# Optimization experiments

Hardware: AMD Instinct MI355X
Metric: run time of the kernel (lower is better)

Reference implementation:

```python
import jax, jax.numpy as jnp
from jax import lax
import numpy as np


def _conv2d(x, w, pad, dil=1):
    return lax.conv_general_dilated(x, w, (1, 1), [(pad, pad), (pad, pad)],
                                    rhs_dilation=(dil, dil),
                                    dimension_numbers=('NCHW', 'OIHW', 'NCHW'))


def _conv1d(x, w):
    # x [B,C,L], w [O,I,K], 'same' padding
    k = w.shape[2]
    return lax.conv_general_dilated(x, w, (1,), [(k // 2, k // 2)],
                                    dimension_numbers=('NCH', 'OIH', 'NCH'))


def _scan_fwd(slices, w):
    # slices [L,B,C,M]; s[i] += relu(conv1d(s[i-1])) for i=1..L-1 (sequential, carries updates)
    def f(c, r):
        n = r + jax.nn.relu(_conv1d(c, w))
        return n, n
    _, out = lax.scan(f, slices[0], slices[1:])
    return jnp.concatenate([slices[:1], out], axis=0)


def _scan_bwd(slices, w):
    # s[i] += relu(conv1d(s[i+1])) for i = L-2 .. 1 (first and last slice untouched)
    def f(c, r):
        n = r + jax.nn.relu(_conv1d(c, w))
        return n, n
    _, out = lax.scan(f, slices[-1], slices[-2:0:-1])
    return jnp.concatenate([slices[:1], out[::-1], slices[-1:]], axis=0)


def _resize_bilinear_ac(x, oh, ow):
    # bilinear, align_corners=True, x [B,C,H,W]
    H, W = x.shape[2], x.shape[3]
    ys = jnp.linspace(0.0, H - 1.0, oh)
    xs = jnp.linspace(0.0, W - 1.0, ow)
    y0 = jnp.floor(ys).astype(jnp.int32); y1 = jnp.minimum(y0 + 1, H - 1)
    x0 = jnp.floor(xs).astype(jnp.int32); x1 = jnp.minimum(x0 + 1, W - 1)
    wy = (ys - y0)[:, None]
    wx = xs - x0
    r = x[:, :, y0, :] * (1.0 - wy) + x[:, :, y1, :] * wy  # [B,C,oh,W]
    return r[:, :, :, x0] * (1.0 - wx) + r[:, :, :, x1] * wx


def reference(x, w11, s11, b11, w12, s12, b12, w21, s21, b21, w22, s22, b22,
              w31, s31, b31, w32, s32, b32, w33, s33, b33,
              w41, s41, b41, w42, s42, b42, w43, s43, b43,
              w51, s51, b51, w52, s52, b52, w53, s53, b53,
              w6, s6, b6, w7, s7, b7, wd, wu, wr, wl, w8, b8,
              fw9, fb9, fw10, fb10):
    def cbr(h, w, s, b, pad=1, dil=1):
        y = _conv2d(h, w, pad, dil)
        return jax.nn.relu(y * s[None, :, None, None] + b[None, :, None, None])

    def mp(h):
        B, C, H, W = h.shape
        return h.reshape(B, C, H // 2, 2, W // 2, 2).max((3, 5))

    x = cbr(x, w11, s11, b11); x = cbr(x, w12, s12, b12); x = mp(x)
    x = cbr(x, w21, s21, b21); x = cbr(x, w22, s22, b22); x = mp(x)
    x = cbr(x, w31, s31, b31); x = cbr(x, w32, s32, b32); x = cbr(x, w33, s33, b33); x = mp(x)
    x = cbr(x, w41, s41, b41); x = cbr(x, w42, s42, b42); x = cbr(x, w43, s43, b43)
    x = cbr(x, w51, s51, b51, pad=2, dil=2)
    x = cbr(x, w52, s52, b52, pad=2, dil=2)
    x = cbr(x, w53, s53, b53, pad=2, dil=2)
    x = cbr(x, w6, s6, b6, pad=4, dil=4)
    x = cbr(x, w7, s7, b7, pad=0)

    # SCNN spatial message passing (down, up over rows; right, left over cols)
    rows = jnp.moveaxis(x, 2, 0)            # [H,B,C,W]
    rows = _scan_fwd(rows, wd[:, :, 0, :])  # down
    rows = _scan_bwd(rows, wu[:, :, 0, :])  # up
    x = jnp.moveaxis(rows, 0, 2)
    cols = jnp.moveaxis(x, 3, 0)            # [W,B,C,H]
    cols = _scan_fwd(cols, wr[:, :, :, 0])  # right
    cols = _scan_bwd(cols, wl[:, :, :, 0])  # left
    x = jnp.moveaxis(cols, 0, 3)

    # dropout2d(p=0.1) treated as identity (deterministic/eval reference)
    x = _conv2d(x, w8, 0) + b8[None, :, None, None]  # [B,5,36,100]

    x1 = jax.nn.softmax(_resize_bilinear_ac(x, 288, 800), axis=1)

    x2 = jax.nn.softmax(x, axis=1)
    B, C, H, W = x2.shape
    x2 = x2.reshape(B, C, H // 2, 2, W // 2, 2).mean((3, 5)).reshape(B, -1)
    x2 = jax.nn.relu(x2 @ fw9.T + fb9)
    x2 = jax.nn.sigmoid(x2 @ fw10.T + fb10)
    return (x1, x2)


def setup_inputs():
    key = jax.random.key(0)
    ks = iter(jax.random.split(key, 80))

    def conv_w(ci, co, kh, kw):
        return jax.random.normal(next(ks), (co, ci, kh, kw), jnp.float32) * np.float32(np.sqrt(2.0 / (ci * kh * kw)))

    def bn(c):
        s = 0.9 + 0.2 * jax.random.uniform(next(ks), (c,), jnp.float32)
        b = 0.1 * jax.random.normal(next(ks), (c,), jnp.float32)
        return s, b

    d = {}
    d['x'] = jax.random.normal(next(ks), (4, 3, 288, 800), jnp.float32)
    specs = [('11', 3, 64), ('12', 64, 64), ('21', 64, 128), ('22', 128, 128),
             ('31', 128, 256), ('32', 256, 256), ('33', 256, 256),
             ('41', 256, 512), ('42', 512, 512), ('43', 512, 512),
             ('51', 512, 512), ('52', 512, 512), ('53', 512, 512)]
    for n, ci, co in specs:
        d['w' + n] = conv_w(ci, co, 3, 3)
        d['s' + n], d['b' + n] = bn(co)
    d['w6'] = conv_w(512, 1024, 3, 3); d['s6'], d['b6'] = bn(1024)
    d['w7'] = conv_w(1024, 128, 1, 1); d['s7'], d['b7'] = bn(128)
    # small scale keeps the 100-step additive recurrence numerically tame
    for n, (kh, kw) in (('wd', (1, 9)), ('wu', (1, 9)), ('wr', (9, 1)), ('wl', (9, 1))):
        d[n] = jax.random.normal(next(ks), (128, 128, kh, kw), jnp.float32) * 0.001
    d['w8'] = conv_w(128, 5, 1, 1)
    d['b8'] = 0.1 * jax.random.normal(next(ks), (5,), jnp.float32)
    d['fw9'] = jax.random.normal(next(ks), (128, 4500), jnp.float32) / np.float32(np.sqrt(4500.0))
    d['fb9'] = jnp.zeros((128,), jnp.float32)
    d['fw10'] = jax.random.normal(next(ks), (4, 128), jnp.float32) / np.float32(np.sqrt(128.0))
    d['fb10'] = jnp.zeros((4,), jnp.float32)
    return d
```

## Files before the change

kernel.cpp:

```cpp
#include <hip/hip_runtime.h>
#include <math.h>


#define NB 4

typedef unsigned short ushort_t;
typedef __attribute__((ext_vector_type(8))) short short8x;
typedef __attribute__((ext_vector_type(4))) float facc4;

static __device__ __forceinline__ ushort_t f2bh(float x) {
    unsigned u = __float_as_uint(x);
    unsigned r = u + 0x7fffu + ((u >> 16) & 1u);
    return (ushort_t)(r >> 16);
}
static __device__ __forceinline__ float bh2f(ushort_t h) {
    return __uint_as_float(((unsigned)h) << 16);
}
static __device__ __forceinline__ void split_store(float v, ushort_t* __restrict__ hi,
                                                   ushort_t* __restrict__ lo, size_t idx) {
    ushort_t h = f2bh(v);
    float l = v - bh2f(h);
    hi[idx] = h;
    lo[idx] = f2bh(l);
}
static __device__ __forceinline__ void ld8f(const float* p, float f[8]) {
    float4 a = *(const float4*)p;
    float4 b = *(const float4*)(p + 4);
    f[0] = a.x; f[1] = a.y; f[2] = a.z; f[3] = a.w;
    f[4] = b.x; f[5] = b.y; f[6] = b.z; f[7] = b.w;
}

__global__ __launch_bounds__(256) void repack_w_k(const float* __restrict__ w, float* __restrict__ wre,
                                                  int O, int IK) {
    int gid = blockIdx.x * 256 + threadIdx.x;
    if (gid >= O * IK) return;
    int o = gid / IK;
    int r = gid - o * IK;
    wre[r * O + o] = w[gid];
}

__global__ __launch_bounds__(256) void conv11_strip_k(const float* __restrict__ X0, const float* __restrict__ W11,
                                                      const float* __restrict__ sc, const float* __restrict__ bi,
                                                      ushort_t* __restrict__ Thi, ushort_t* __restrict__ Tlo, int r0) {
    int gid = blockIdx.x * 256 + threadIdx.x;
    if (gid >= 4 * 20 * 802 * 8) return;
    int c8 = gid & 7;
    int t = gid >> 3;
    int w = t % 802; t /= 802;
    int tr = t % 20;
    int b = t / 20;
    int gr = r0 - 1 + tr;
    int gc = w - 1;
    size_t obase = (((size_t)b * 20 + tr) * 802 + w) * 64 + c8 * 8;
    if (gr < 0 || gr >= 288 || gc < 0 || gc >= 800) {
#pragma unroll
        for (int j = 0; j < 8; ++j) { Thi[obase + j] = 0; Tlo[obase + j] = 0; }
        return;
    }
    float acc[8];
#pragma unroll
    for (int j = 0; j < 8; ++j) acc[j] = 0.f;
#pragma unroll
    for (int ci = 0; ci < 3; ++ci) {
        const float* inc = X0 + (size_t)(b * 3 + ci) * 288 * 800;
#pragma unroll
        for (int kh = 0; kh < 3; ++kh) {
            int ih = gr + kh - 1;
            if (ih < 0 || ih >= 288) continue;
#pragma unroll
            for (int kw = 0; kw < 3; ++kw) {
                int iw = gc + kw - 1;
                if (iw < 0 || iw >= 800) continue;
                float v = inc[ih * 800 + iw];
                float wf[8];
                ld8f(W11 + (ci * 9 + kh * 3 + kw) * 64 + c8 * 8, wf);
#pragma unroll
                for (int j = 0; j < 8; ++j) acc[j] = fmaf(v, wf[j], acc[j]);
            }
        }
    }
#pragma unroll
    for (int j = 0; j < 8; ++j) {
        int n = c8 * 8 + j;
        float r = acc[j] * sc[n] + bi[n];
        r = r > 0.f ? r : 0.f;
        split_store(r, Thi, Tlo, obase + j);
    }
}

__global__ __launch_bounds__(256) void repack_wmfma_k(const float* __restrict__ w, ushort_t* __restrict__ whi,
                                                      ushort_t* __restrict__ wlo, int N, int Cin, int taps) {
    int gid = blockIdx.x * 256 + threadIdx.x;
    if (gid >= N * Cin * taps) return;
    int o = gid / (Cin * taps);
    int r = gid - o * Cin * taps;
    int i = r / taps;
    int t = r - i * taps;
    float x = w[gid];
    size_t d = ((size_t)t * N + o) * Cin + i;
    ushort_t h = f2bh(x);
    whi[d] = h;
    wlo[d] = f2bh(x - bh2f(h));
}

__global__ __launch_bounds__(256) void vpool2_k(const ushort_t* __restrict__ shi, const ushort_t* __restrict__ slo,
                                                ushort_t* __restrict__ dhi, ushort_t* __restrict__ dlo,
                                                int Hs, int Wp, int C, int Hop, int Wop, int pad, int pr0) {
    int total = 4 * (Hs >> 1) * Wp * C;
    int gid = blockIdx.x * 256 + threadIdx.x;
    if (gid >= total) return;
    int c = gid % C;
    int t = gid / C;
    int w = t % Wp; t /= Wp;
    int hp = t % (Hs >> 1);
    int b = t / (Hs >> 1);
    size_t a0 = (((size_t)b * Hs + 2 * hp) * Wp + w) * C + c;
    size_t a1 = a0 + (size_t)Wp * C;
    float v0 = bh2f(shi[a0]) + bh2f(slo[a0]);
    float v1 = bh2f(shi[a1]) + bh2f(slo[a1]);
    float v = fmaxf(v0, v1);
    size_t d = (((size_t)b * Hop + pr0 + hp + pad) * Wop + (w + pad)) * C + c;
    split_store(v, dhi, dlo, d);
}

template <int MODE, int NJ>
__global__ __launch_bounds__(256) void mfma_conv_k(
    const ushort_t* __restrict__ Ahi, const ushort_t* __restrict__ Alo,
    const ushort_t* __restrict__ Whi, const ushort_t* __restrict__ Wlo,
    const float* __restrict__ sc, const float* __restrict__ bi,
    ushort_t* __restrict__ Ohi, ushort_t* __restrict__ Olo, float* __restrict__ Fo,
    int M, int Wimg, int HS, int h0,
    int HpIn, int WpIn, int Cin, int ih0, int iph, int ipw, int dil, int taps,
    int N, int obst, int oh0, int oph, int opw, int WpOut) {
    constexpr int NT = NJ * 32;
    __shared__ ushort_t sA0[128 * 40], sA1[128 * 40];
    __shared__ ushort_t sB0[NT * 40], sB1[NT * 40];

    int tid = threadIdx.x;
    int m0 = blockIdx.x * 128;
    int n0 = blockIdx.y * NT;

    int ar = tid >> 1;
    int ah = (tid & 1) * 16;
    int am = m0 + ar;
    if (am >= M) am = M - 1;
    int aw = am % Wimg;
    int t1 = am / Wimg;
    int ahh = h0 + t1 % HS;
    int ab = t1 / HS;

    int br, bhh, bpl;
    if (NJ == 4) {
        br = tid >> 1; bhh = (tid & 1) * 16; bpl = 2;
    } else {
        int bp = tid >> 7;
        int bidx = tid & 127;
        br = bidx >> 1; bhh = (bidx & 1) * 16; bpl = bp;
    }

    int wid = tid >> 6, lane = tid & 63;
    int moff = (wid >> 1) * 64;
    int noff = (wid & 1) * (NJ * 16);
    int lm = lane & 15, quad = lane >> 4;

    facc4 acc[4][NJ];
#pragma unroll
    for (int i = 0; i < 4; ++i)
#pragma unroll
        for (int j = 0; j < NJ; ++j) acc[i][j] = (facc4)(0.f);

    for (int t = 0; t < taps; ++t) {
        int dh = 0, dw = 0;
        if (taps == 9) {
            dh = (t / 3 - 1) * dil;
            dw = (t % 3 - 1) * dil;
        }
        size_t aoff = (((size_t)ab * HpIn + (ahh - ih0 + iph + dh)) * WpIn + (aw + ipw + dw)) * Cin + ah;
        size_t boff0 = ((size_t)t * N + (n0 + br)) * Cin + bhh;
        for (int k0 = 0; k0 < Cin; k0 += 32) {
            {
                const ushort_t* p = Ahi + aoff + k0;
                uint4 v0 = *(const uint4*)p;
                uint4 v1 = *(const uint4*)(p + 8);
                *(uint4*)&sA0[ar * 40 + ah] = v0;
                *(uint4*)&sA0[ar * 40 + ah + 8] = v1;
                const ushort_t* q = Alo + aoff + k0;
                uint4 w0 = *(const uint4*)q;
                uint4 w1 = *(const uint4*)(q + 8);
                *(uint4*)&sA1[ar * 40 + ah] = w0;
                *(uint4*)&sA1[ar * 40 + ah + 8] = w1;
            }
            if (NJ == 4) {
                const ushort_t* p = Whi + boff0 + k0;
                uint4 v0 = *(const uint4*)p;
                uint4 v1 = *(const uint4*)(p + 8);
                *(uint4*)&sB0[br * 40 + bhh] = v0;
                *(uint4*)&sB0[br * 40 + bhh + 8] = v1;
                const ushort_t* q = Wlo + boff0 + k0;
                uint4 w0 = *(const uint4*)q;
                uint4 w1 = *(const uint4*)(q + 8);
                *(uint4*)&sB1[br * 40 + bhh] = w0;
                *(uint4*)&sB1[br * 40 + bhh + 8] = w1;
            } else {
                const ushort_t* p = (bpl ? Wlo : Whi) + boff0 + k0;
                uint4 v0 = *(const uint4*)p;
                uint4 v1 = *(const uint4*)(p + 8);
                ushort_t* dst = bpl ? sB1 : sB0;
                *(uint4*)&dst[br * 40 + bhh] = v0;
                *(uint4*)&dst[br * 40 + bhh + 8] = v1;
            }
            __syncthreads();
            short8x afh[4], afl[4], bfh[NJ], bfl[NJ];
#pragma unroll
            for (int mi = 0; mi < 4; ++mi) {
                int base = (moff + mi * 16 + lm) * 40 + quad * 8;
                afh[mi] = *(const short8x*)&sA0[base];
                afl[mi] = *(const short8x*)&sA1[base];
            }
#pragma unroll
            for (int nj = 0; nj < NJ; ++nj) {
                int base = (noff + nj * 16 + lm) * 40 + quad * 8;
                bfh[nj] = *(const short8x*)&sB0[base];
                bfl[nj] = *(const short8x*)&sB1[base];
            }
#pragma unroll
            for (int mi = 0; mi < 4; ++mi)
#pragma unroll
                for (int nj = 0; nj < NJ; ++nj) {
                    acc[mi][nj] = __builtin_amdgcn_mfma_f32_16x16x32_bf16(afh[mi], bfh[nj], acc[mi][nj], 0, 0, 0);
                    acc[mi][nj] = __builtin_amdgcn_mfma_f32_16x16x32_bf16(afl[mi], bfh[nj], acc[mi][nj], 0, 0, 0);
                    acc[mi][nj] = __builtin_amdgcn_mfma_f32_16x16x32_bf16(afh[mi], bfl[nj], acc[mi][nj], 0, 0, 0);
                }
            __syncthreads();
        }
    }

#pragma unroll
    for (int mi = 0; mi < 4; ++mi)
#pragma unroll
        for (int nj = 0; nj < NJ; ++nj) {
            int nglob = n0 + noff + nj * 16 + lm;
            float s = sc[nglob];
            float bb = bi[nglob];
            if (MODE == 1) {
#pragma unroll
                for (int rg = 0; rg < 4; rg += 2) {
                    int mg = m0 + moff + mi * 16 + quad * 4 + rg;
                    if (mg >= M) continue;
                    float v0 = acc[mi][nj][rg] * s + bb;
                    v0 = v0 > 0.f ? v0 : 0.f;
                    float v1 = acc[mi][nj][rg + 1] * s + bb;
                    v1 = v1 > 0.f ? v1 : 0.f;
                    float v = fmaxf(v0, v1);
                    int wq = mg % Wimg;
                    int tq = mg / Wimg;
                    int hq = h0 + tq % HS;
                    int bq = tq / HS;
                    size_t a = ((size_t)bq * obst + (size_t)(hq - oh0) * WpOut + (wq >> 1)) * N + nglob;
                    split_store(v, Ohi, Olo, a);
                }
            } else {
#pragma unroll
                for (int rg = 0; rg < 4; ++rg) {
                    int mg = m0 + moff + mi * 16 + quad * 4 + rg;
                    if (mg >= M) continue;
                    float v = acc[mi][nj][rg] * s + bb;
                    v = v > 0.f ? v : 0.f;
                    int wq = mg % Wimg;
                    int tq = mg / Wimg;
                    int hq = h0 + tq % HS;
                    int bq = tq / HS;
                    if (MODE == 0) {
                        size_t a = ((size_t)bq * obst + (size_t)(hq - oh0 + oph) * WpOut + (wq + opw)) * N + nglob;
                        split_store(v, Ohi, Olo, a);
                    } else {
                        size_t a = (((size_t)bq * N + nglob) * HS + (hq - h0)) * Wimg + wq;
                        Fo[a] = v;
                    }
                }
            }
        }
}

__global__ __launch_bounds__(256) void repack_scan_k(const float* __restrict__ w, float* __restrict__ wre) {
    int gid = blockIdx.x * 256 + threadIdx.x;
    if (gid >= 128 * 128 * 9) return;
    int o = gid / 1152;
    int r = gid - o * 1152;
    wre[r * 128 + o] = w[gid];
}

__global__ __launch_bounds__(256) void scan_row_k(float* __restrict__ F, const float* __restrict__ wsc, int hp, int hc) {
    __shared__ float sm[128 * 12];
    int b = blockIdx.x / 25;
    int w0 = (blockIdx.x % 25) * 4;
    int tid = threadIdx.x;
    const float* Fp = F + ((size_t)(b * 128) * 36 + hp) * 100;
    for (int i = tid; i < 1536; i += 256) {
        int ci = i / 12;
        int j = i - ci * 12;
        int iw = w0 - 4 + j;
        sm[i] = (iw >= 0 && iw < 100) ? Fp[(size_t)ci * 3600 + iw] : 0.f;
    }
    __syncthreads();
    int o = tid & 127;
    int half = tid >> 7;
    float a0 = 0.f, a1 = 0.f;
    for (int ci = 0; ci < 128; ++ci) {
        const float* s = sm + ci * 12 + half * 2;
        const float* wp = wsc + ci * 9 * 128 + o;
#pragma unroll
        for (int k = 0; k < 9; ++k) {
            float wt = wp[k * 128];
            a0 = fmaf(s[k], wt, a0);
            a1 = fmaf(s[k + 1], wt, a1);
        }
    }
    int w = w0 + half * 2;
    float* outp = F + ((size_t)(b * 128 + o) * 36 + hc) * 100 + w;
    outp[0] += a0 > 0.f ? a0 : 0.f;
    outp[1] += a1 > 0.f ? a1 : 0.f;
}

__global__ __launch_bounds__(256) void scan_colT_k(float* __restrict__ FT, const float* __restrict__ wsc, int wp_, int wc) {
    __shared__ float sm[128 * 12];
    int b = blockIdx.x / 9;
    int h0 = (blockIdx.x % 9) * 4;
    int tid = threadIdx.x;
    const float* Fp = FT + (size_t)(b * 128) * 3600 + (size_t)wp_ * 36;
    for (int i = tid; i < 1536; i += 256) {
        int ci = i / 12;
        int j = i - ci * 12;
        int ih = h0 - 4 + j;
        sm[i] = (ih >= 0 && ih < 36) ? Fp[(size_t)ci * 3600 + ih] : 0.f;
    }
    __syncthreads();
    int o = tid & 127;
    int half = tid >> 7;
    float a0 = 0.f, a1 = 0.f;
    for (int ci = 0; ci < 128; ++ci) {
        const float* s = sm + ci * 12 + half * 2;
        const float* wp = wsc + ci * 9 * 128 + o;
#pragma unroll
        for (int k = 0; k < 9; ++k) {
            float wt = wp[k * 128];
            a0 = fmaf(s[k], wt, a0);
            a1 = fmaf(s[k + 1], wt, a1);
        }
    }
    int h = h0 + half * 2;
    float* outp = FT + ((size_t)(b * 128 + o) * 100 + wc) * 36 + h;
    outp[0] += a0 > 0.f ? a0 : 0.f;
    outp[1] += a1 > 0.f ? a1 : 0.f;
}

__global__ __launch_bounds__(256) void transpose_fwd_k(const float* __restrict__ F, float* __restrict__ FT) {
    int gid = blockIdx.x * 256 + threadIdx.x;
    if (gid >= 4 * 128 * 3600) return;
    int h = gid % 36;
    int t = gid / 36;
    int w = t % 100;
    int bc = t / 100;
    FT[gid] = F[(size_t)bc * 3600 + h * 100 + w];
}
__global__ __launch_bounds__(256) void transpose_bwd_k(const float* __restrict__ FT, float* __restrict__ F) {
    int gid = blockIdx.x * 256 + threadIdx.x;
    if (gid >= 4 * 128 * 3600) return;
    int w = gid % 100;
    int t = gid / 100;
    int h = t % 36;
    int bc = t / 36;
    F[gid] = FT[(size_t)bc * 3600 + w * 36 + h];
}

__global__ __launch_bounds__(256) void conv8_k(const float* __restrict__ F, const float* __restrict__ w8,
                                               const float* __restrict__ b8, float* __restrict__ G) {
    int gid = blockIdx.x * 256 + threadIdx.x;
    if (gid >= NB * 3600) return;
    int hw = gid % 3600;
    int b = gid / 3600;
    float acc[5];
#pragma unroll
    for (int c = 0; c < 5; ++c) acc[c] = b8[c];
    const float* Fb = F + (size_t)b * 128 * 3600 + hw;
    for (int ci = 0; ci < 128; ++ci) {
        float v = Fb[(size_t)ci * 3600];
#pragma unroll
        for (int c = 0; c < 5; ++c) acc[c] = fmaf(v, w8[c * 128 + ci], acc[c]);
    }
#pragma unroll
    for (int c = 0; c < 5; ++c) G[(size_t)(b * 5 + c) * 3600 + hw] = acc[c];
}

__global__ __launch_bounds__(256) void resize_softmax_k(const float* __restrict__ G, float* __restrict__ out) {
    int gid = blockIdx.x * 256 + threadIdx.x;
    if (gid >= NB * 288 * 800) return;
    int ox = gid % 800;
    int t = gid / 800;
    int oy = t % 288;
    int b = t / 288;
    float fy = oy * (35.0f / 287.0f);
    int y0 = (int)fy; if (y0 > 34) y0 = 34;
    int y1 = y0 + 1;
    float wy = fy - y0;
    float fx = ox * (99.0f / 799.0f);
    int x0 = (int)fx; if (x0 > 98) x0 = 98;
    int x1 = x0 + 1;
    float wx = fx - x0;
    const float* Gb = G + (size_t)b * 5 * 3600;
    float v[5];
    float m = -1e30f;
#pragma unroll
    for (int c = 0; c < 5; ++c) {
        const float* Gc = Gb + (size_t)c * 3600;
        float a = Gc[y0 * 100 + x0] * (1.f - wx) + Gc[y0 * 100 + x1] * wx;
        float bb = Gc[y1 * 100 + x0] * (1.f - wx) + Gc[y1 * 100 + x1] * wx;
        v[c] = a * (1.f - wy) + bb * wy;
        m = fmaxf(m, v[c]);
    }
    float sum = 0.f;
#pragma unroll
    for (int c = 0; c < 5; ++c) { v[c] = expf(v[c] - m); sum += v[c]; }
    float inv = 1.f / sum;
#pragma unroll
    for (int c = 0; c < 5; ++c) out[((size_t)(b * 5 + c) * 288 + oy) * 800 + ox] = v[c] * inv;
}

__global__ __launch_bounds__(256) void pool_softmax_k(const float* __restrict__ G, float* __restrict__ P) {
    int gid = blockIdx.x * 256 + threadIdx.x;
    if (gid >= NB * 18 * 50) return;
    int pw = gid % 50;
    int t = gid / 50;
    int ph = t % 18;
    int b = t / 18;
    float s5[5] = {0.f, 0.f, 0.f, 0.f, 0.f};
    const float* Gb = G + (size_t)b * 5 * 3600;
#pragma unroll
    for (int dy = 0; dy < 2; ++dy) {
#pragma unroll
        for (int dx = 0; dx < 2; ++dx) {
            int hw = (2 * ph + dy) * 100 + (2 * pw + dx);
            float v[5], m = -1e30f, sum = 0.f;
#pragma unroll
            for (int c = 0; c < 5; ++c) { v[c] = Gb[(size_t)c * 3600 + hw]; m = fmaxf(m, v[c]); }
#pragma unroll
            for (int c = 0; c < 5; ++c) { v[c] = expf(v[c] - m); sum += v[c]; }
            float inv = 1.f / sum;
#pragma unroll
            for (int c = 0; c < 5; ++c) s5[c] += v[c] * inv;
        }
    }
#pragma unroll
    for (int c = 0; c < 5; ++c) P[b * 4500 + c * 900 + ph * 50 + pw] = s5[c] * 0.25f;
}

__global__ __launch_bounds__(256) void fc1_k(const float* __restrict__ P, const float* __restrict__ fw9,
                                             const float* __restrict__ fb9, float* __restrict__ H1) {
    int wid = blockIdx.x * 4 + (threadIdx.x >> 6);
    int lane = threadIdx.x & 63;
    if (wid >= 512) return;
    int b = wid >> 7;
    int o = wid & 127;
    const float* wr = fw9 + (size_t)o * 4500;
    const float* pr = P + b * 4500;
    float acc = 0.f;
    for (int i = lane; i < 4500; i += 64) acc = fmaf(wr[i], pr[i], acc);
    for (int s = 32; s > 0; s >>= 1) acc += __shfl_down(acc, s, 64);
    if (lane == 0) {
        float r = acc + fb9[o];
        H1[b * 128 + o] = r > 0.f ? r : 0.f;
    }
}

__global__ __launch_bounds__(64) void fc2_k(const float* __restrict__ H1, const float* __restrict__ fw10,
                                            const float* __restrict__ fb10, float* __restrict__ dout) {
    int t = threadIdx.x;
    if (t >= 16) return;
    int b = t >> 2;
    int o = t & 3;
    float acc = fb10[o];
    for (int i = 0; i < 128; ++i) acc = fmaf(H1[b * 128 + i], fw10[o * 128 + i], acc);
    dout[4608000 + t] = 1.f / (1.f + expf(-acc));
}

static inline int ceildiv(int a, int b) { return (a + b - 1) / b; }

extern "C" void kernel_launch(void* const* d_in, const int* in_sizes, int n_in,
                              void* d_out, int out_size, void* d_ws, size_t ws_size,
                              hipStream_t stream) {
    (void)in_sizes; (void)n_in; (void)out_size; (void)ws_size;
    char* U = (char*)d_ws;
    char* V = U + 19000064;

    float* W11f = (float*)(U);
    ushort_t* WM12 = (ushort_t*)(U + 8192);
    ushort_t* WM21 = (ushort_t*)(U + 155648);
    ushort_t* WM22 = (ushort_t*)(U + 450560);
    ushort_t* T1hi = (ushort_t*)(U + 1050624);
    ushort_t* T1lo = (ushort_t*)(U + 1050624 + 8212480);
    ushort_t* T3hi = (ushort_t*)(U + 1050624);
    ushort_t* T3lo = (ushort_t*)(U + 1050624 + 8232960);
    ushort_t* WMa = (ushort_t*)(U);
    ushort_t* WMb = (ushort_t*)(U + 4718592);
    float* WSC = (float*)(U);
    float* G = (float*)(U + 2359296);
    float* P = (float*)(U + 2647296);
    float* H1 = (float*)(U + 2719296);

    ushort_t* Xhi = (ushort_t*)(V);
    ushort_t* Xlo = (ushort_t*)(V + 15306752);
    ushort_t* S1hi = (ushort_t*)(V + 30613504);
    ushort_t* S1lo = (ushort_t*)(V + 60663808);
    ushort_t* T2hi = (ushort_t*)(V + 90714112);
    ushort_t* T2lo = (ushort_t*)(V + 90714112 + 3686400);
    ushort_t* Yhi = (ushort_t*)(V + 30613504);
    ushort_t* Ylo = (ushort_t*)(V + 61227008);
    ushort_t* Zhi = (ushort_t*)(V + 91840512);
    ushort_t* Zlo = (ushort_t*)(V + 97632256);
    ushort_t* HPhi = (ushort_t*)(V);
    ushort_t* HPlo = (ushort_t*)(V + 14745600);
    ushort_t* PAhi = (ushort_t*)(V + 30613504);
    ushort_t* PAlo = (ushort_t*)(V + 40345600);
    ushort_t* SBhi = (ushort_t*)(V + 50077696);
    ushort_t* SBlo = (ushort_t*)(V + 69541888);
    ushort_t* SAhi = (ushort_t*)(V);
    ushort_t* SAlo = (ushort_t*)(V + 19464192);
    ushort_t* C6hi = (ushort_t*)(V + 38928384);
    ushort_t* C6lo = (ushort_t*)(V + 68419584);
    float* F = (float*)(V);
    float* FT = (float*)(V + 7372800);

    const float* X0 = (const float*)d_in[0];
    auto din = [&](int i) { return (const float*)d_in[i]; };
    auto wm_lo = [&](ushort_t* base, int taps, int N, int C) { return base + (size_t)taps * N * C; };

    repack_w_k<<<ceildiv(27 * 64, 256), 256, 0, stream>>>(din(1), W11f, 64, 27);
    repack_wmfma_k<<<ceildiv(64 * 64 * 9, 256), 256, 0, stream>>>(din(4), WM12, wm_lo(WM12, 9, 64, 64), 64, 64, 9);
    hipMemsetAsync(V + 30613504, 0, 60100608, stream);
    for (int s = 0; s < 16; ++s) {
        int r0 = s * 18;
        conv11_strip_k<<<2005, 256, 0, stream>>>(X0, W11f, din(2), din(3), T1hi, T1lo, r0);
        mfma_conv_k<1, 2><<<dim3(450, 1), 256, 0, stream>>>(
            T1hi, T1lo, WM12, wm_lo(WM12, 9, 64, 64), din(5), din(6), T2hi, T2lo, nullptr,
            57600, 800, 18, r0, 20, 802, 64, r0, 1, 1, 1, 9, 64, 18 * 400, r0, 0, 0, 400);
        vpool2_k<<<ceildiv(4 * 9 * 400 * 64, 256), 256, 0, stream>>>(
            T2hi, T2lo, S1hi, S1lo, 18, 400, 64, 146, 402, 1, r0 / 2);
    }
    repack_wmfma_k<<<ceildiv(128 * 64 * 9, 256), 256, 0, stream>>>(din(7), WM21, wm_lo(WM21, 9, 128, 64), 128, 64, 9);
    repack_wmfma_k<<<ceildiv(128 * 128 * 9, 256), 256, 0, stream>>>(din(10), WM22, wm_lo(WM22, 9, 128, 128), 128, 128, 9);
    hipMemsetAsync(V, 0, 30613504, stream);
    for (int s = 0; s < 8; ++s) {
        int r0 = s * 18;
        int hstart = r0 - 1 < 0 ? 0 : r0 - 1;
        int hend = r0 + 19 > 144 ? 144 : r0 + 19;
        int rows = hend - hstart;
        int M21 = 4 * rows * 400;
        hipMemsetAsync(U + 1050624, 0, 16465920, stream);
        mfma_conv_k<0, 4><<<dim3(ceildiv(M21, 128), 1), 256, 0, stream>>>(
            S1hi, S1lo, WM21, wm_lo(WM21, 9, 128, 64), din(8), din(9), T3hi, T3lo, nullptr,
            M21, 400, rows, hstart, 146, 402, 64, 0, 1, 1, 1, 9, 128, 20 * 402, r0 - 1, 0, 1, 402);
        mfma_conv_k<1, 4><<<dim3(225, 1), 256, 0, stream>>>(
            T3hi, T3lo, WM22, wm_lo(WM22, 9, 128, 128), din(11), din(12), T2hi, T2lo, nullptr,
            28800, 400, 18, r0, 20, 402, 128, r0 - 1, 0, 1, 1, 9, 128, 18 * 200, r0, 0, 0, 200);
        vpool2_k<<<ceildiv(4 * 9 * 200 * 128, 256), 256, 0, stream>>>(
            T2hi, T2lo, Xhi, Xlo, 18, 200, 128, 74, 202, 1, r0 / 2);
    }

    repack_wmfma_k<<<ceildiv(256 * 128 * 9, 256), 256, 0, stream>>>(din(13), WMa, wm_lo(WMa, 9, 256, 128), 256, 128, 9);
    hipMemsetAsync(V + 30613504, 0, 61227008, stream);
    mfma_conv_k<0, 4><<<dim3(450, 2), 256, 0, stream>>>(
        Xhi, Xlo, WMa, wm_lo(WMa, 9, 256, 128), din(14), din(15), Yhi, Ylo, nullptr,
        57600, 200, 72, 0, 74, 202, 128, 0, 1, 1, 1, 9, 256, 74 * 202, 0, 1, 1, 202);
    repack_wmfma_k<<<ceildiv(256 * 256 * 9, 256), 256, 0, stream>>>(din(16), WMa, wm_lo(WMa, 9, 256, 256), 256, 256, 9);
    repack_wmfma_k<<<ceildiv(256 * 256 * 9, 256), 256, 0, stream>>>(din(19), WMb, wm_lo(WMb, 9, 256, 256), 256, 256, 9);
    for (int s = 0; s < 6; ++s) {
        int h0s = s * 12;
        int hstart = h0s - 1 < 0 ? 0 : h0s - 1;
        int hend = h0s + 13 > 72 ? 72 : h0s + 13;
        int rows = hend - hstart;
        int M32 = 4 * rows * 200;
        hipMemsetAsync(V + 91840512, 0, 11583488, stream);
        mfma_conv_k<0, 4><<<dim3(ceildiv(M32, 128), 2), 256, 0, stream>>>(
            Yhi, Ylo, WMa, wm_lo(WMa, 9, 256, 256), din(17), din(18), Zhi, Zlo, nullptr,
            M32, 200, rows, hstart, 74, 202, 256, 0, 1, 1, 1, 9, 256, 14 * 202, h0s - 1, 0, 1, 202);
        mfma_conv_k<1, 4><<<dim3(75, 2), 256, 0, stream>>>(
            Zhi, Zlo, WMb, wm_lo(WMb, 9, 256, 256), din(20), din(21), HPhi, HPlo, nullptr,
            9600, 200, 12, h0s, 14, 202, 256, h0s - 1, 0, 1, 1, 9, 256, 72 * 100, 0, 0, 0, 100);
    }
    hipMemsetAsync(V + 30613504, 0, 19464192, stream);
    vpool2_k<<<ceildiv(4 * 36 * 100 * 256, 256), 256, 0, stream>>>(
        HPhi, HPlo, PAhi, PAlo, 72, 100, 256, 44, 108, 4, 0);

    struct L { int wi, si, bi, dil; };
    static const L l45[5] = {{25, 26, 27, 1}, {28, 29, 30, 1}, {31, 32, 33, 2}, {34, 35, 36, 2}, {37, 38, 39, 2}};
    repack_wmfma_k<<<ceildiv(512 * 256 * 9, 256), 256, 0, stream>>>(din(22), WMa, wm_lo(WMa, 9, 512, 256), 512, 256, 9);
    hipMemsetAsync(V + 50077696, 0, 38928384, stream);
    mfma_conv_k<0, 4><<<dim3(113, 4), 256, 0, stream>>>(
        PAhi, PAlo, WMa, wm_lo(WMa, 9, 512, 256), din(23), din(24), SBhi, SBlo, nullptr,
        14400, 100, 36, 0, 44, 108, 256, 0, 4, 4, 1, 9, 512, 44 * 108, 0, 4, 4, 108);
    hipMemsetAsync(V, 0, 38928384, stream);
    for (int i = 0; i < 5; ++i) {
        const L& L0 = l45[i];
        repack_wmfma_k<<<ceildiv(512 * 512 * 9, 256), 256, 0, stream>>>(din(L0.wi), WMa, wm_lo(WMa, 9, 512, 512), 512, 512, 9);
        const ushort_t* ih = (i & 1) ? SAhi : SBhi;
        const ushort_t* il = (i & 1) ? SAlo : SBlo;
        ushort_t* oh = (i & 1) ? SBhi : SAhi;
        ushort_t* ol = (i & 1) ? SBlo : SAlo;
        mfma_conv_k<0, 4><<<dim3(113, 4), 256, 0, stream>>>(
            ih, il, WMa, wm_lo(WMa, 9, 512, 512), din(L0.si), din(L0.bi), oh, ol, nullptr,
            14400, 100, 36, 0, 44, 108, 512, 0, 4, 4, L0.dil, 9, 512, 44 * 108, 0, 4, 4, 108);
    }
    repack_wmfma_k<<<ceildiv(1024 * 512 * 9, 256), 256, 0, stream>>>(din(40), WMa, wm_lo(WMa, 9, 1024, 512), 1024, 512, 9);
    mfma_conv_k<0, 4><<<dim3(113, 8), 256, 0, stream>>>(
        SAhi, SAlo, WMa, wm_lo(WMa, 9, 1024, 512), din(41), din(42), C6hi, C6lo, nullptr,
        14400, 100, 36, 0, 44, 108, 512, 0, 4, 4, 4, 9, 1024, 3600, 0, 0, 0, 100);
    repack_wmfma_k<<<ceildiv(128 * 1024, 256), 256, 0, stream>>>(din(43), WMa, wm_lo(WMa, 1, 128, 1024), 128, 1024, 1);
    mfma_conv_k<2, 4><<<dim3(113, 1), 256, 0, stream>>>(
        C6hi, C6lo, WMa, wm_lo(WMa, 1, 128, 1024), din(44), din(45), nullptr, nullptr, F,
        14400, 100, 36, 0, 36, 100, 1024, 0, 0, 0, 1, 1, 128, 0, 0, 0, 0, 0);

    for (int j = 0; j < 4; ++j)
        repack_scan_k<<<576, 256, 0, stream>>>(din(46 + j), WSC + (size_t)j * 147456);
    for (int h = 1; h <= 35; ++h)
        scan_row_k<<<100, 256, 0, stream>>>(F, WSC + 0 * 147456, h - 1, h);
    for (int h = 34; h >= 1; --h)
        scan_row_k<<<100, 256, 0, stream>>>(F, WSC + 1 * 147456, h + 1, h);
    transpose_fwd_k<<<7200, 256, 0, stream>>>(F, FT);
    for (int w = 1; w <= 99; ++w)
        scan_colT_k<<<36, 256, 0, stream>>>(FT, WSC + 2 * (size_t)147456, w - 1, w);
    for (int w = 98; w >= 1; --w)
        scan_colT_k<<<36, 256, 0, stream>>>(FT, WSC + 3 * (size_t)147456, w + 1, w);
    transpose_bwd_k<<<7200, 256, 0, stream>>>(FT, F);

    conv8_k<<<ceildiv(NB * 3600, 256), 256, 0, stream>>>(F, din(50), din(51), G);
    resize_softmax_k<<<ceildiv(NB * 288 * 800, 256), 256, 0, stream>>>(G, (float*)d_out);
    pool_softmax_k<<<ceildiv(NB * 18 * 50, 256), 256, 0, stream>>>(G, P);
    fc1_k<<<128, 256, 0, stream>>>(P, din(52), din(53), H1);
    fc2_k<<<1, 64, 0, stream>>>(H1, din(54), din(55), (float*)d_out);
}
```

Measured before the change: 11.05 ms.

## Prefetch next K-chunk into registers while computing current chunk in conv GEMM

Flattens the tap and K-chunk loops into one loop and software-pipelines the global loads. The next chunk's A and B tiles are loaded into registers while MFMAs run on the tile already in shared memory. This is meant to hide global memory latency behind compute. It costs extra registers per thread, which may lower occupancy.

```diff
diff --git a/kernel.cpp b/kernel.cpp
--- a/kernel.cpp
+++ b/kernel.cpp
@@ -169,70 +169,85 @@
 #pragma unroll
         for (int j = 0; j < NJ; ++j) acc[i][j] = (facc4)(0.f);
 
-    for (int t = 0; t < taps; ++t) {
+    const long abase = ((long)ab * HpIn + (ahh - ih0 + iph)) * WpIn + (aw + ipw);
+    const long bbase = (long)(n0 + br) * Cin + bhh;
+    const int nch = Cin >> 5;
+    const int total = taps * nch;
+
+    uint4 rA[4];
+    uint4 rB[4];
+
+    auto issue_loads = [&](int t, int k0) {
         int dh = 0, dw = 0;
         if (taps == 9) {
             dh = (t / 3 - 1) * dil;
             dw = (t % 3 - 1) * dil;
         }
-        size_t aoff = (((size_t)ab * HpIn + (ahh - ih0 + iph + dh)) * WpIn + (aw + ipw + dw)) * Cin + ah;
-        size_t boff0 = ((size_t)t * N + (n0 + br)) * Cin + bhh;
-        for (int k0 = 0; k0 < Cin; k0 += 32) {
-            {
-                const ushort_t* p = Ahi + aoff + k0;
-                uint4 v0 = *(const uint4*)p;
-                uint4 v1 = *(const uint4*)(p + 8);
-                *(uint4*)&sA0[ar * 40 + ah] = v0;
-                *(uint4*)&sA0[ar * 40 + ah + 8] = v1;
-                const ushort_t* q = Alo + aoff + k0;
-                uint4 w0 = *(const uint4*)q;
-                uint4 w1 = *(const uint4*)(q + 8);
-                *(uint4*)&sA1[ar * 40 + ah] = w0;
-                *(uint4*)&sA1[ar * 40 + ah + 8] = w1;
+        long ao = (abase + (long)dh * WpIn + dw) * Cin + ah + k0;
+        const ushort_t* p = Ahi + ao;
+        rA[0] = *(const uint4*)p;
+        rA[1] = *(const uint4*)(p + 8);
+        const ushort_t* q = Alo + ao;
+        rA[2] = *(const uint4*)q;
+        rA[3] = *(const uint4*)(q + 8);
+        long bo = (long)t * N * Cin + bbase + k0;
+        if (NJ == 4) {
+            const ushort_t* pb = Whi + bo;
+            rB[0] = *(const uint4*)pb;
+            rB[1] = *(const uint4*)(pb + 8);
+            const ushort_t* qb = Wlo + bo;
+            rB[2] = *(const uint4*)qb;
+            rB[3] = *(const uint4*)(qb + 8);
+        } else {
+            const ushort_t* pb = (bpl ? Wlo : Whi) + bo;
+            rB[0] = *(const uint4*)pb;
+            rB[1] = *(const uint4*)(pb + 8);
+        }
+    };
+
+    issue_loads(0, 0);
+    int tn = 0, kn = 0;
+    for (int i = 0; i < total; ++i) {
+        ++kn;
+        if (kn == nch) { kn = 0; ++tn; }
+        __syncthreads();
+        *(uint4*)&sA0[ar * 40 + ah] = rA[0];
+        *(uint4*)&sA0[ar * 40 + ah + 8] = rA[1];
+        *(uint4*)&sA1[ar * 40 + ah] = rA[2];
+        *(uint4*)&sA1[ar * 40 + ah + 8] = rA[3];
+        if (NJ == 4) {
+            *(uint4*)&sB0[br * 40 + bhh] = rB[0];
+            *(uint4*)&sB0[br * 40 + bhh + 8] = rB[1];
+            *(uint4*)&sB1[br * 40 + bhh] = rB[2];
+            *(uint4*)&sB1[br * 40 + bhh + 8] = rB[3];
+        } else {
+            ushort_t* dst = bpl ? sB1 : sB0;
+            *(uint4*)&dst[br * 40 + bhh] = rB[0];
+            *(uint4*)&dst[br * 40 + bhh + 8] = rB[1];
+        }
+        __syncthreads();
+        if (i + 1 < total) issue_loads(tn, kn * 32);
+        short8x afh[4], afl[4], bfh[NJ], bfl[NJ];
+#pragma unroll
+        for (int mi = 0; mi < 4; ++mi) {
+            int base = (moff + mi * 16 + lm) * 40 + quad * 8;
+            afh[mi] = *(const short8x*)&sA0[base];
+            afl[mi] = *(const short8x*)&sA1[base];
+        }
+#pragma unroll
+        for (int nj = 0; nj < NJ; ++nj) {
+            int base = (noff + nj * 16 + lm) * 40 + quad * 8;
+            bfh[nj] = *(const short8x*)&sB0[base];
+            bfl[nj] = *(const short8x*)&sB1[base];
+        }
+#pragma unroll
+        for (int mi = 0; mi < 4; ++mi)
+#pragma unroll
+            for (int nj = 0; nj < NJ; ++nj) {
+                acc[mi][nj] = __builtin_amdgcn_mfma_f32_16x16x32_bf16(afh[mi], bfh[nj], acc[mi][nj], 0, 0, 0);
+                acc[mi][nj] = __builtin_amdgcn_mfma_f32_16x16x32_bf16(afl[mi], bfh[nj], acc[mi][nj], 0, 0, 0);
+                acc[mi][nj] = __builtin_amdgcn_mfma_f32_16x16x32_bf16(afh[mi], bfl[nj], acc[mi][nj], 0, 0, 0);
             }
-            if (NJ == 4) {
-                const ushort_t* p = Whi + boff0 + k0;
-                uint4 v0 = *(const uint4*)p;
-                uint4 v1 = *(const uint4*)(p + 8);
-                *(uint4*)&sB0[br * 40 + bhh] = v0;
-                *(uint4*)&sB0[br * 40 + bhh + 8] = v1;
-                const ushort_t* q = Wlo + boff0 + k0;
-                uint4 w0 = *(const uint4*)q;
-                uint4 w1 = *(const uint4*)(q + 8);
-                *(uint4*)&sB1[br * 40 + bhh] = w0;
-                *(uint4*)&sB1[br * 40 + bhh + 8] = w1;
-            } else {
-                const ushort_t* p = (bpl ? Wlo : Whi) + boff0 + k0;
-                uint4 v0 = *(const uint4*)p;
-                uint4 v1 = *(const uint4*)(p + 8);
-                ushort_t* dst = bpl ? sB1 : sB0;
-                *(uint4*)&dst[br * 40 + bhh] = v0;
-                *(uint4*)&dst[br * 40 + bhh + 8] = v1;
-            }
-            __syncthreads();
-            short8x afh[4], afl[4], bfh[NJ], bfl[NJ];
-#pragma unroll
-            for (int mi = 0; mi < 4; ++mi) {
-                int base = (moff + mi * 16 + lm) * 40 + quad * 8;
-                afh[mi] = *(const short8x*)&sA0[base];
-                afl[mi] = *(const short8x*)&sA1[base];
-            }
-#pragma unroll
-            for (int nj = 0; nj < NJ; ++nj) {
-                int base = (noff + nj * 16 + lm) * 40 + quad * 8;
-                bfh[nj] = *(const short8x*)&sB0[base];
-                bfl[nj] = *(const short8x*)&sB1[base];
-            }
-#pragma unroll
-            for (int mi = 0; mi < 4; ++mi)
-#pragma unroll
-                for (int nj = 0; nj < NJ; ++nj) {
-                    acc[mi][nj] = __builtin_amdgcn_mfma_f32_16x16x32_bf16(afh[mi], bfh[nj], acc[mi][nj], 0, 0, 0);
-                    acc[mi][nj] = __builtin_amdgcn_mfma_f32_16x16x32_bf16(afl[mi], bfh[nj], acc[mi][nj], 0, 0, 0);
-                    acc[mi][nj] = __builtin_amdgcn_mfma_f32_16x16x32_bf16(afh[mi], bfl[nj], acc[mi][nj], 0, 0, 0);
-                }
-            __syncthreads();
-        }
     }
 
 #pragma unroll
```

Measured after the change: 18.08 ms. 1.64x slower.

## Load conv MFMA tiles via direct global-to-LDS async loads with swizzled layout

Applied to the files above, without the earlier changes.

The implicit-GEMM conv kernel now fills shared memory with global_load_lds (global-to-LDS without passing through registers). Each wavefront owns one plane (A hi/lo, B hi/lo). The padded 40-stride LDS layout is replaced by a dense 32-stride layout with an XOR-like chunk swizzle to avoid bank conflicts. Pixel offsets are precomputed per thread, and Cin is assumed to be a power of two for shift-based addressing. This cuts register staging and VGPR pressure, but relies on the vmcnt handling around __syncthreads and assumes Cin is a multiple of 32 and a power of two.

```diff
diff --git a/kernel.cpp b/kernel.cpp
--- a/kernel.cpp
+++ b/kernel.cpp
@@ -28,6 +28,11 @@
     float4 b = *(const float4*)(p + 4);
     f[0] = a.x; f[1] = a.y; f[2] = a.z; f[3] = a.w;
     f[4] = b.x; f[5] = b.y; f[6] = b.z; f[7] = b.w;
+}
+static __device__ __forceinline__ void async_ld(const ushort_t* g, ushort_t* l) {
+    __builtin_amdgcn_global_load_lds(
+        (const __attribute__((address_space(1))) unsigned int*)(const void*)g,
+        (__attribute__((address_space(3))) unsigned int*)(void*)l, 16, 0, 0);
 }
 
 __global__ __launch_bounds__(256) void repack_w_k(const float* __restrict__ w, float* __restrict__ wre,
@@ -133,35 +138,48 @@
     int HpIn, int WpIn, int Cin, int ih0, int iph, int ipw, int dil, int taps,
     int N, int obst, int oh0, int oph, int opw, int WpOut) {
     constexpr int NT = NJ * 32;
-    __shared__ ushort_t sA0[128 * 40], sA1[128 * 40];
-    __shared__ ushort_t sB0[NT * 40], sB1[NT * 40];
+    __shared__ ushort_t sA0[128 * 32], sA1[128 * 32];
+    __shared__ ushort_t sB0[NT * 32], sB1[NT * 32];
 
     int tid = threadIdx.x;
     int m0 = blockIdx.x * 128;
     int n0 = blockIdx.y * NT;
-
-    int ar = tid >> 1;
-    int ah = (tid & 1) * 16;
-    int am = m0 + ar;
-    if (am >= M) am = M - 1;
-    int aw = am % Wimg;
-    int t1 = am / Wimg;
-    int ahh = h0 + t1 % HS;
-    int ab = t1 / HS;
-
-    int br, bhh, bpl;
-    if (NJ == 4) {
-        br = tid >> 1; bhh = (tid & 1) * 16; bpl = 2;
-    } else {
-        int bp = tid >> 7;
-        int bidx = tid & 127;
-        br = bidx >> 1; bhh = (bidx & 1) * 16; bpl = bp;
-    }
 
     int wid = tid >> 6, lane = tid & 63;
     int moff = (wid >> 1) * 64;
     int noff = (wid & 1) * (NJ * 16);
     int lm = lane & 15, quad = lane >> 4;
+
+    const int lgC = 31 - __clz(Cin);
+    int lr16 = lane >> 2;
+    int lq = ((lane & 3) - ((lr16 >> 1) & 3)) & 3;
+    int qoff = lq * 8;
+
+    const ushort_t* gplane;
+    ushort_t* lplane;
+    if (wid == 0)      { gplane = Ahi; lplane = sA0; }
+    else if (wid == 1) { gplane = Alo; lplane = sA1; }
+    else if (wid == 2) { gplane = Whi; lplane = sB0; }
+    else               { gplane = Wlo; lplane = sB1; }
+    bool isA = (wid < 2);
+
+    int pix[8];
+    if (isA) {
+#pragma unroll
+        for (int j = 0; j < 8; ++j) {
+            int R = j * 16 + lr16;
+            int am = m0 + R;
+            if (am >= M) am = M - 1;
+            int aw2 = am % Wimg;
+            int tt = am / Wimg;
+            int hh = h0 + tt % HS;
+            int bb2 = tt / HS;
+            pix[j] = (bb2 * HpIn + (hh - ih0 + iph)) * WpIn + (aw2 + ipw);
+        }
+    }
+    int nbase = n0 + lr16;
+
+    int cA8 = ((quad + ((lm >> 1) & 3)) & 3) * 8;
 
     facc4 acc[4][NJ];
 #pragma unroll
@@ -175,51 +193,33 @@
             dh = (t / 3 - 1) * dil;
             dw = (t % 3 - 1) * dil;
         }
-        size_t aoff = (((size_t)ab * HpIn + (ahh - ih0 + iph + dh)) * WpIn + (aw + ipw + dw)) * Cin + ah;
-        size_t boff0 = ((size_t)t * N + (n0 + br)) * Cin + bhh;
+        int dhw = dh * WpIn + dw;
+        long btap = (long)t * N;
         for (int k0 = 0; k0 < Cin; k0 += 32) {
-            {
-                const ushort_t* p = Ahi + aoff + k0;
-                uint4 v0 = *(const uint4*)p;
-                uint4 v1 = *(const uint4*)(p + 8);
-                *(uint4*)&sA0[ar * 40 + ah] = v0;
-                *(uint4*)&sA0[ar * 40 + ah + 8] = v1;
-                const ushort_t* q = Alo + aoff + k0;
-                uint4 w0 = *(const uint4*)q;
-                uint4 w1 = *(const uint4*)(q + 8);
-                *(uint4*)&sA1[ar * 40 + ah] = w0;
-                *(uint4*)&sA1[ar * 40 + ah + 8] = w1;
-            }
-            if (NJ == 4) {
-                const ushort_t* p = Whi + boff0 + k0;
-                uint4 v0 = *(const uint4*)p;
-                uint4 v1 = *(const uint4*)(p + 8);
-                *(uint4*)&sB0[br * 40 + bhh] = v0;
-                *(uint4*)&sB0[br * 40 + bhh + 8] = v1;
-                const ushort_t* q = Wlo + boff0 + k0;
-                uint4 w0 = *(const uint4*)q;
-                uint4 w1 = *(const uint4*)(q + 8);
-                *(uint4*)&sB1[br * 40 + bhh] = w0;
-                *(uint4*)&sB1[br * 40 + bhh + 8] = w1;
+            if (isA) {
+#pragma unroll
+                for (int j = 0; j < 8; ++j) {
+                    long ga = ((long)(pix[j] + dhw) << lgC) + (qoff + k0);
+                    async_ld(gplane + ga, lplane + j * 512);
+                }
             } else {
-                const ushort_t* p = (bpl ? Wlo : Whi) + boff0 + k0;
-                uint4 v0 = *(const uint4*)p;
-                uint4 v1 = *(const uint4*)(p + 8);
-                ushort_t* dst = bpl ? sB1 : sB0;
-                *(uint4*)&dst[br * 40 + bhh] = v0;
-                *(uint4*)&dst[br * 40 + bhh + 8] = v1;
+#pragma unroll
+                for (int j = 0; j < NJ * 2; ++j) {
+                    long gb = ((btap + nbase + j * 16) << lgC) + (qoff + k0);
+                    async_ld(gplane + gb, lplane + j * 512);
+                }
             }
             __syncthreads();
             short8x afh[4], afl[4], bfh[NJ], bfl[NJ];
 #pragma unroll
             for (int mi = 0; mi < 4; ++mi) {
-                int base = (moff + mi * 16 + lm) * 40 + quad * 8;
+                int base = (moff + mi * 16 + lm) * 32 + cA8;
                 afh[mi] = *(const short8x*)&sA0[base];
                 afl[mi] = *(const short8x*)&sA1[base];
             }
 #pragma unroll
             for (int nj = 0; nj < NJ; ++nj) {
-                int base = (noff + nj * 16 + lm) * 40 + quad * 8;
+                int base = (noff + nj * 16 + lm) * 32 + cA8;
                 bfh[nj] = *(const short8x*)&sB0[base];
                 bfl[nj] = *(const short8x*)&sB1[base];
             }
```

Result: faster. 10.50 ms (-5.0%).
